# Performance work log

Hardware: AMD Instinct MI355X
Metric: run time of the kernel (lower is better)

## Reference

```python
import jax, jax.numpy as jnp
from jax import lax
import numpy as np

IN_C, OUT_C, K, N_SPLIT = 256, 256, 3, 4
N_LEGO = int(OUT_C * 0.25)          # 64
BASIC_C = IN_C // N_SPLIT           # 64


def setup_inputs() -> dict:
    key = jax.random.key(0)
    k1, k2, k3, k4 = jax.random.split(key, 4)
    x = jax.random.normal(k1, (32, IN_C, 56, 56), dtype=jnp.float32)
    # kaiming-normal-ish initialization of parameters
    lego = jax.random.normal(k2, (N_LEGO, BASIC_C, K, 1), dtype=jnp.float32) * np.sqrt(2.0 / (BASIC_C * K))
    aux_coefficients = jax.random.normal(k3, (N_SPLIT, OUT_C, N_LEGO, 1, 1), dtype=jnp.float32) * np.sqrt(2.0 / N_LEGO)
    aux_combination = jax.random.normal(k4, (N_SPLIT, OUT_C, N_LEGO, 1, 1), dtype=jnp.float32) * np.sqrt(2.0 / N_LEGO)
    return {"x": x, "lego": lego, "aux_coefficients": aux_coefficients, "aux_combination": aux_combination}


def reference(x, lego, aux_coefficients, aux_combination):
    n_split, out_c, n_lego = aux_combination.shape[:3]
    bc = lego.shape[1]
    # one-hot selection: each (split, out_channel) picks exactly one lego feature
    idx = jnp.argmax(aux_combination[..., 0, 0], axis=2)              # (n_split, out_c)
    proxy = jax.nn.one_hot(idx, n_lego, dtype=x.dtype)                # (n_split, out_c, n_lego)
    W = aux_coefficients[..., 0, 0] * proxy                           # (n_split, out_c, n_lego)
    out = 0.0
    for i in range(n_split):
        xi = x[:, i * bc:(i + 1) * bc]                                # (B, bc, H, W)
        feat = lax.conv_general_dilated(
            xi, lego, window_strides=(3, 1), padding=((1, 1), (1, 1)),
            dimension_numbers=("NCHW", "OIHW", "NCHW"))               # (B, n_lego, Ho, Wo)
        out = out + jnp.einsum("bnhw,on->bohw", feat, W[i])
    return out
```

## Files before the change

### kernel.cpp

```cpp
#include <hip/hip_runtime.h>

#define INC    256
#define HIN    56
#define WIN    56
#define HOUT   19
#define WOUT   58
#define KTOT   768

typedef short frag8 __attribute__((ext_vector_type(8)));
typedef float f32x4 __attribute__((ext_vector_type(4)));

static __device__ __forceinline__ unsigned short f2bf(float f) {
    unsigned u = __float_as_uint(f);
    u += 0x7fffu + ((u >> 16) & 1u);
    return (unsigned short)(u >> 16);
}

__global__ __launch_bounds__(256) void prep_weff(
    const float* __restrict__ lego,
    const float* __restrict__ coefs,
    const float* __restrict__ comb,
    unsigned short* __restrict__ Asw)
{
    __shared__ int   idxS[4];
    __shared__ float cofS[4];
    const int t  = threadIdx.x;
    const int kx = blockIdx.x;
    const int o  = blockIdx.y;
    const int wv = t >> 6, l = t & 63;

    float v  = comb[(wv * 256 + o) * 64 + l];
    int   bi = l;
    #pragma unroll
    for (int off = 32; off >= 1; off >>= 1) {
        float ov = __shfl_xor(v, off, 64);
        int   oi = __shfl_xor(bi, off, 64);
        if (ov > v || (ov == v && oi < bi)) { v = ov; bi = oi; }
    }
    if (l == 0) {
        idxS[wv] = bi;
        cofS[wv] = coefs[(wv * 256 + o) * 64 + bi];
    }
    __syncthreads();

    const int k  = kx * 256 + t;
    const int kh = k >> 8, c = k & 255;
    const int i  = c >> 6, cl = c & 63;
    float w = cofS[i] * lego[idxS[i] * 192 + cl * 3 + kh];

    const int o_tile = o >> 4, m = o & 15;
    const int ks = k >> 5, kc = (k >> 3) & 3, j = k & 7;
    Asw[((((size_t)o_tile * 24 + ks) * 64) + kc * 16 + m) * 8 + j] = f2bf(w);
}

__global__ __launch_bounds__(256) void conv_mfma(
    const float* __restrict__ x,
    const unsigned short* __restrict__ Asw,
    float* __restrict__ out)
{
    __shared__ unsigned short Xs[24 * 2 * 64 * 8];

    const int t  = threadIdx.x;
    const int wh = blockIdx.x;
    const int h  = blockIdx.y;
    const int b  = blockIdx.z;

    {
        const float* xb = x + (size_t)b * (INC * HIN * WIN);
        const int w   = t & 31;
        const int kg  = t >> 5;
        const int col = wh * 32 - 1 + w;
        const bool colok = (unsigned)col < (unsigned)WIN;
        const int wtile = w >> 4;
        const int lbase = (w & 15);
        const int rowbase = 3 * h - 1;

        for (int s = 0; s < 3; ++s) {
            const int ks  = kg * 3 + s;
            const int kh  = ks >> 3;
            const int row = rowbase + kh;
            const bool rowok = (unsigned)row < (unsigned)HIN;
            const float* xrow = xb + (size_t)row * WIN + col;
            const int cbase = (ks & 7) * 32;
            #pragma unroll
            for (int kc = 0; kc < 4; ++kc) {
                union { frag8 f; unsigned short u[8]; } pk;
                #pragma unroll
                for (int j = 0; j < 8; ++j) {
                    int c = cbase + kc * 8 + j;
                    float v = 0.f;
                    if (colok && rowok) v = xrow[(size_t)c * (HIN * WIN)];
                    pk.u[j] = f2bf(v);
                }
                *(frag8*)&Xs[(((ks * 2 + wtile) * 64) + kc * 16 + lbase) * 8] = pk.f;
            }
        }
    }
    __syncthreads();

    const int l  = t & 63;
    const int lo = l & 15;
    const int hi = l >> 4;
    const int wv = t >> 6;

    f32x4 acc[4][2];
    #pragma unroll
    for (int ot = 0; ot < 4; ++ot)
        #pragma unroll
        for (int nt = 0; nt < 2; ++nt)
            acc[ot][nt] = (f32x4){0.f, 0.f, 0.f, 0.f};

    const frag8* Af = (const frag8*)Asw + ((size_t)(wv * 4) * 24) * 64 + l;
    const frag8* Xf = (const frag8*)Xs + l;

    #pragma unroll 8
    for (int ks = 0; ks < 24; ++ks) {
        frag8 b0 = Xf[(ks * 2) * 64];
        frag8 b1 = Xf[(ks * 2 + 1) * 64];
        #pragma unroll
        for (int ot = 0; ot < 4; ++ot) {
            frag8 a = Af[(ot * 24 + ks) * 64];
            acc[ot][0] = __builtin_amdgcn_mfma_f32_16x16x32_bf16(a, b0, acc[ot][0], 0, 0, 0);
            acc[ot][1] = __builtin_amdgcn_mfma_f32_16x16x32_bf16(a, b1, acc[ot][1], 0, 0, 0);
        }
    }

    const int wb = wh * 32;
    const int obase = wv * 64;
    #pragma unroll
    for (int ot = 0; ot < 4; ++ot) {
        #pragma unroll
        for (int nt = 0; nt < 2; ++nt) {
            int wcol = wb + nt * 16 + lo;
            if (wcol < WOUT) {
                #pragma unroll
                for (int r = 0; r < 4; ++r) {
                    int o = obase + ot * 16 + hi * 4 + r;
                    out[((size_t)(b * 256 + o) * HOUT + h) * WOUT + wcol] = acc[ot][nt][r];
                }
            }
        }
    }
}

extern "C" void kernel_launch(void* const* d_in, const int* in_sizes, int n_in,
                              void* d_out, int out_size, void* d_ws, size_t ws_size,
                              hipStream_t stream) {
    const float* x     = (const float*)d_in[0];
    const float* lego  = (const float*)d_in[1];
    const float* coefs = (const float*)d_in[2];
    const float* comb  = (const float*)d_in[3];
    float* out = (float*)d_out;

    unsigned short* Asw = (unsigned short*)d_ws;

    prep_weff<<<dim3(3, 256), 256, 0, stream>>>(lego, coefs, comb, Asw);
    conv_mfma<<<dim3(2, HOUT, 32), 256, 0, stream>>>(x, Asw, out);
}
```

Baseline: 209.0 us.

## Split conv K-dimension staging into two halves with smaller LDS and register prefetch

The input tile is now staged into shared memory in two chunks of 12 k-steps instead of all 24 at once, which halves the LDS footprint. Launch bounds now request 5 blocks per SM to raise occupancy. The MFMA loop software-prefetches the next A and B fragments into registers. The aim is more resident blocks to hide global-load latency, at the cost of an extra barrier pair per chunk and higher register pressure from the prefetch buffers.

```diff
diff --git a/kernel.cpp b/kernel.cpp
--- a/kernel.cpp
+++ b/kernel.cpp
@@ -53,50 +53,17 @@
     Asw[((((size_t)o_tile * 24 + ks) * 64) + kc * 16 + m) * 8 + j] = f2bf(w);
 }
 
-__global__ __launch_bounds__(256) void conv_mfma(
+__global__ __launch_bounds__(256, 5) void conv_mfma(
     const float* __restrict__ x,
     const unsigned short* __restrict__ Asw,
     float* __restrict__ out)
 {
-    __shared__ unsigned short Xs[24 * 2 * 64 * 8];
+    __shared__ unsigned short Xs[12 * 2 * 64 * 8];
 
     const int t  = threadIdx.x;
     const int wh = blockIdx.x;
     const int h  = blockIdx.y;
     const int b  = blockIdx.z;
-
-    {
-        const float* xb = x + (size_t)b * (INC * HIN * WIN);
-        const int w   = t & 31;
-        const int kg  = t >> 5;
-        const int col = wh * 32 - 1 + w;
-        const bool colok = (unsigned)col < (unsigned)WIN;
-        const int wtile = w >> 4;
-        const int lbase = (w & 15);
-        const int rowbase = 3 * h - 1;
-
-        for (int s = 0; s < 3; ++s) {
-            const int ks  = kg * 3 + s;
-            const int kh  = ks >> 3;
-            const int row = rowbase + kh;
-            const bool rowok = (unsigned)row < (unsigned)HIN;
-            const float* xrow = xb + (size_t)row * WIN + col;
-            const int cbase = (ks & 7) * 32;
-            #pragma unroll
-            for (int kc = 0; kc < 4; ++kc) {
-                union { frag8 f; unsigned short u[8]; } pk;
-                #pragma unroll
-                for (int j = 0; j < 8; ++j) {
-                    int c = cbase + kc * 8 + j;
-                    float v = 0.f;
-                    if (colok && rowok) v = xrow[(size_t)c * (HIN * WIN)];
-                    pk.u[j] = f2bf(v);
-                }
-                *(frag8*)&Xs[(((ks * 2 + wtile) * 64) + kc * 16 + lbase) * 8] = pk.f;
-            }
-        }
-    }
-    __syncthreads();
 
     const int l  = t & 63;
     const int lo = l & 15;
@@ -110,19 +77,67 @@
         for (int nt = 0; nt < 2; ++nt)
             acc[ot][nt] = (f32x4){0.f, 0.f, 0.f, 0.f};
 
+    const float* xb = x + (size_t)b * (INC * HIN * WIN);
+    const int w     = t & 31;
+    const int kg    = t >> 5;
+    const int col   = wh * 32 - 1 + w;
+    const bool colok = (unsigned)col < (unsigned)WIN;
+    const int wtile = w >> 4;
+    const int lbase = w & 15;
+    const int rowbase = 3 * h - 1;
+
     const frag8* Af = (const frag8*)Asw + ((size_t)(wv * 4) * 24) * 64 + l;
     const frag8* Xf = (const frag8*)Xs + l;
 
-    #pragma unroll 8
-    for (int ks = 0; ks < 24; ++ks) {
-        frag8 b0 = Xf[(ks * 2) * 64];
-        frag8 b1 = Xf[(ks * 2 + 1) * 64];
+    for (int c2 = 0; c2 < 2; ++c2) {
+        #pragma unroll
+        for (int q = 0; q < 6; ++q) {
+            int p   = kg * 6 + q;
+            int ksl = p >> 2, kc = p & 3;
+            int kgl = c2 * 384 + ksl * 32 + kc * 8;
+            int kh  = kgl >> 8, c0 = kgl & 255;
+            int row = rowbase + kh;
+            bool ok = colok && ((unsigned)row < (unsigned)HIN);
+            const float* xp = xb + (size_t)c0 * (HIN * WIN) + row * WIN + col;
+            union { frag8 f; unsigned short u[8]; } pk;
+            #pragma unroll
+            for (int j = 0; j < 8; ++j) {
+                float v = ok ? xp[(size_t)j * (HIN * WIN)] : 0.f;
+                pk.u[j] = f2bf(v);
+            }
+            *(frag8*)&Xs[(((ksl * 2 + wtile) * 64) + kc * 16 + lbase) * 8] = pk.f;
+        }
+        __syncthreads();
+
+        const int ksb = c2 * 12;
+        frag8 a[4], an[4], b0, b1, b0n, b1n;
+        #pragma unroll
+        for (int ot = 0; ot < 4; ++ot) a[ot] = Af[(ot * 24 + ksb) * 64];
+        b0 = Xf[0];
+        b1 = Xf[64];
+
+        #pragma unroll
+        for (int ks = 0; ks < 11; ++ks) {
+            #pragma unroll
+            for (int ot = 0; ot < 4; ++ot) an[ot] = Af[(ot * 24 + ksb + ks + 1) * 64];
+            b0n = Xf[((ks + 1) * 2) * 64];
+            b1n = Xf[((ks + 1) * 2 + 1) * 64];
+
+            #pragma unroll
+            for (int ot = 0; ot < 4; ++ot) {
+                acc[ot][0] = __builtin_amdgcn_mfma_f32_16x16x32_bf16(a[ot], b0, acc[ot][0], 0, 0, 0);
+                acc[ot][1] = __builtin_amdgcn_mfma_f32_16x16x32_bf16(a[ot], b1, acc[ot][1], 0, 0, 0);
+            }
+            #pragma unroll
+            for (int ot = 0; ot < 4; ++ot) a[ot] = an[ot];
+            b0 = b0n; b1 = b1n;
+        }
         #pragma unroll
         for (int ot = 0; ot < 4; ++ot) {
-            frag8 a = Af[(ot * 24 + ks) * 64];
-            acc[ot][0] = __builtin_amdgcn_mfma_f32_16x16x32_bf16(a, b0, acc[ot][0], 0, 0, 0);
-            acc[ot][1] = __builtin_amdgcn_mfma_f32_16x16x32_bf16(a, b1, acc[ot][1], 0, 0, 0);
+            acc[ot][0] = __builtin_amdgcn_mfma_f32_16x16x32_bf16(a[ot], b0, acc[ot][0], 0, 0, 0);
+            acc[ot][1] = __builtin_amdgcn_mfma_f32_16x16x32_bf16(a[ot], b1, acc[ot][1], 0, 0, 0);
         }
+        __syncthreads();
     }
 
     const int wb = wh * 32;
```

Measured after the change: 194.2 us. 1.08x faster.
